# Kernel optimization log

Hardware: AMD Instinct MI355X
Metric: run time of the kernel (lower is better)

## Reference

```python
import jax, jax.numpy as jnp
import numpy as np

LN_EPS = 1e-5


def _ln(x, g, b):
    m = jnp.mean(x, axis=-1, keepdims=True)
    v = jnp.mean((x - m) ** 2, axis=-1, keepdims=True)
    return (x - m) / jnp.sqrt(v + LN_EPS) * g + b


def setup_inputs() -> dict:
    key = jax.random.key(0)
    ks = jax.random.split(key, 8)
    B, N, S, D, T = 16, 64, 2048, 1024, 768

    def xavier(k, shape):
        fan_in, fan_out = shape
        lim = (6.0 / (fan_in + fan_out)) ** 0.5
        return jax.random.uniform(k, shape, minval=-lim, maxval=lim, dtype=jnp.float32)

    return {
        "prev_states": jax.random.normal(ks[0], (B, N, D), dtype=jnp.float32),
        "input_tokens": jax.random.normal(ks[1], (B, S, T), dtype=jnp.float32),
        # input_projection (token_dim -> state_dim)
        "W_proj": xavier(ks[2], (T, D)),
        "b_proj": jnp.zeros((D,), jnp.float32),
        # three LayerNorms
        "g_state": jnp.ones((D,), jnp.float32), "beta_state": jnp.zeros((D,), jnp.float32),
        "g_input": jnp.ones((D,), jnp.float32), "beta_input": jnp.zeros((D,), jnp.float32),
        "g_out": jnp.ones((D,), jnp.float32), "beta_out": jnp.zeros((D,), jnp.float32),
        # GRU gates (2D -> D); update-gate bias initialized to -1 as in the module
        "W_u": xavier(ks[3], (2 * D, D)), "b_u": jnp.full((D,), -1.0, jnp.float32),
        "W_r": xavier(ks[4], (2 * D, D)), "b_r": jnp.zeros((D,), jnp.float32),
        "W_n": xavier(ks[5], (2 * D, D)), "b_n": jnp.zeros((D,), jnp.float32),
    }


def reference(prev_states, input_tokens, W_proj, b_proj,
              g_state, beta_state, g_input, beta_input, g_out, beta_out,
              W_u, b_u, W_r, b_r, W_n, b_n):
    D = prev_states.shape[-1]
    # project tokens to state dim: (B,S,D)
    tok = input_tokens @ W_proj + b_proj
    # attention routing (routing_weights=None path)
    scores = jnp.einsum('bnd,bsd->bns', prev_states, tok) / jnp.sqrt(jnp.float32(D))
    attn = jax.nn.softmax(scores, axis=-1)
    routed = jnp.einsum('bns,bsd->bnd', attn, tok)  # (B,N,D)
    # GRU-style gated update, vectorized over the num_states axis
    ps_n = _ln(prev_states, g_state, beta_state)
    in_n = _ln(routed, g_input, beta_input)
    concat = jnp.concatenate([ps_n, in_n], axis=-1)  # (B,N,2D)
    u = jax.nn.sigmoid(concat @ W_u + b_u)
    r = jax.nn.sigmoid(concat @ W_r + b_r)
    reset_in = jnp.concatenate([r * ps_n, in_n], axis=-1)
    cand = jnp.tanh(reset_in @ W_n + b_n)  # dropout is identity in eval
    new_state = (1.0 - u) * prev_states + u * cand
    return _ln(new_state, g_out, beta_out)
```

## Files before the change

### kernel.cpp

```cpp
#include <hip/hip_runtime.h>
#include <stdint.h>

typedef __attribute__((ext_vector_type(4))) float floatx4;
typedef __attribute__((ext_vector_type(8))) short shortx8;

#define LN_EPS 1e-5f

__device__ __forceinline__ unsigned short f2b(float f) {
  unsigned u = __builtin_bit_cast(unsigned, f);
  u = (u + 0x7FFFu + ((u >> 16) & 1u)) >> 16;
  return (unsigned short)u;
}
__device__ __forceinline__ float b2f(unsigned short h) {
  return __builtin_bit_cast(float, (unsigned)h << 16);
}

__device__ __forceinline__ void g2l16(const unsigned short* g, unsigned short* l) {
  __builtin_amdgcn_global_load_lds(
      (const __attribute__((address_space(1))) unsigned int*)g,
      (__attribute__((address_space(3))) unsigned int*)l, 16, 0, 0);
}

__device__ __forceinline__ float wave_sum(float v) {
#pragma unroll
  for (int o = 32; o; o >>= 1) v += __shfl_down(v, o, 64);
  return v;
}
__device__ __forceinline__ float block_sum(float v, float* s) {
  v = wave_sum(v);
  __syncthreads();
  if ((threadIdx.x & 63) == 0) s[threadIdx.x >> 6] = v;
  __syncthreads();
  return s[0] + s[1] + s[2] + s[3];
}

__global__ __launch_bounds__(256) void k_transpose4(
    const float* __restrict__ Wu, const float* __restrict__ Wr,
    const float* __restrict__ Wn, const float* __restrict__ Wp,
    unsigned short* __restrict__ Wtur, unsigned short* __restrict__ Wtn,
    unsigned short* __restrict__ Wtp) {
  __shared__ float tile[32][33];
  const int which = blockIdx.z;
  const float* in;
  unsigned short* out;
  int K;
  if (which == 0)      { in = Wu; out = Wtur;              K = 2048; }
  else if (which == 1) { in = Wr; out = Wtur + 1024 * 2048; K = 2048; }
  else if (which == 2) { in = Wn; out = Wtn;               K = 2048; }
  else                 { in = Wp; out = Wtp;               K = 768;  }
  const int N = 1024;
  const int k0 = blockIdx.x * 32, n0 = blockIdx.y * 32;
  if (k0 >= K) return;
  const int tx = threadIdx.x & 31, ty = threadIdx.x >> 5;
#pragma unroll
  for (int i = 0; i < 32; i += 8)
    tile[ty + i][tx] = in[(long)(k0 + ty + i) * N + n0 + tx];
  __syncthreads();
#pragma unroll
  for (int i = 0; i < 32; i += 8)
    out[(long)(n0 + ty + i) * K + k0 + tx] = f2b(tile[tx][ty + i]);
}

__global__ __launch_bounds__(256) void k_cvt3(
    const float* __restrict__ prev, unsigned short* __restrict__ psb,
    const float* __restrict__ toks, unsigned short* __restrict__ tokb,
    const float* __restrict__ wp, unsigned short* __restrict__ wpb,
    float* __restrict__ rs) {
  if (blockIdx.x == 0) {
    floatx4 z = {0.f, 0.f, 0.f, 0.f};
    *(floatx4*)(rs + threadIdx.x * 4) = z;
  }
  const long chunk = (long)blockIdx.x * 256 + threadIdx.x;
  const float* src;
  unsigned short* dst;
  long i;
  if (chunk < 262144) { src = prev; dst = psb; i = chunk * 4; }
  else if (chunk < 6553600) { src = toks; dst = tokb; i = (chunk - 262144) * 4; }
  else { src = wp; dst = wpb; i = (chunk - 6553600) * 4; }
  floatx4 v = *(const floatx4*)(src + i);
  unsigned short t4[4];
#pragma unroll
  for (int j = 0; j < 4; j++) t4[j] = f2b(v[j]);
  *(uint2*)(dst + i) = *(uint2*)t4;
}

__global__ __launch_bounds__(256) void k_gemm64(
    const unsigned short* __restrict__ A, long sAb, int lda,
    const unsigned short* __restrict__ Bt, long sBb, int ldb,
    int K,
    const float* __restrict__ bias, const float* __restrict__ bias2,
    float scale, int mode,
    void* __restrict__ out, int ldc, long sCb,
    unsigned short* __restrict__ out2,
    const unsigned short* __restrict__ aux_psn,
    const float* __restrict__ aux_u, const float* __restrict__ aux_prev,
    float* __restrict__ rs) {
  __shared__ unsigned short As[2][64 * 64];
  __shared__ unsigned short Bs[2][64 * 64];
  const int tid = threadIdx.x;
  const int wave = tid >> 6, lane = tid & 63;
  const int b = blockIdx.z;
  const int m0 = blockIdx.x * 64, n0 = blockIdx.y * 64;
  const int wm = wave & 1, wn = wave >> 1;
  const int l16 = lane & 15, quad = lane >> 4;
  const int srow8 = lane >> 3;
  const int c8 = ((lane & 7) ^ srow8) * 8;
  const unsigned short* Ab = A + (long)b * sAb;
  const unsigned short* Bb = Bt + (long)b * sBb;

  const unsigned short* gA[2];
  const unsigned short* gB[2];
  int lAoff[2], lBoff[2];
#pragma unroll
  for (int j = 0; j < 2; j++) {
    const int rb = wave * 16 + j * 8;
    gA[j] = Ab + (long)(m0 + rb + srow8) * lda + c8;
    gB[j] = Bb + (long)(n0 + rb + srow8) * ldb + c8;
    lAoff[j] = rb * 64;
    lBoff[j] = rb * 64;
  }
  int offA[2][2], offB[2][2];
#pragma unroll
  for (int ks = 0; ks < 2; ks++)
#pragma unroll
    for (int i = 0; i < 2; i++) {
      int r = wm * 32 + i * 16 + l16;
      offA[ks][i] = r * 64 + (((ks * 4 + quad) ^ (r & 7)) * 8);
      r = wn * 32 + i * 16 + l16;
      offB[ks][i] = r * 64 + (((ks * 4 + quad) ^ (r & 7)) * 8);
    }

  floatx4 acc[2][2] = {};

#pragma unroll
  for (int j = 0; j < 2; j++) {
    g2l16(gA[j], &As[0][lAoff[j]]);
    g2l16(gB[j], &Bs[0][lBoff[j]]);
  }
  __syncthreads();

  const int nt = K >> 6;
  for (int t = 0; t < nt; t++) {
    const int cur = t & 1;
    if (t + 1 < nt) {
      const int kn = (t + 1) << 6;
#pragma unroll
      for (int j = 0; j < 2; j++) {
        g2l16(gA[j] + kn, &As[cur ^ 1][lAoff[j]]);
        g2l16(gB[j] + kn, &Bs[cur ^ 1][lBoff[j]]);
      }
    }
#pragma unroll
    for (int ks = 0; ks < 2; ks++) {
      shortx8 af[2], bf[2];
#pragma unroll
      for (int i = 0; i < 2; i++) af[i] = *(const shortx8*)&As[cur][offA[ks][i]];
#pragma unroll
      for (int j = 0; j < 2; j++) bf[j] = *(const shortx8*)&Bs[cur][offB[ks][j]];
#pragma unroll
      for (int i = 0; i < 2; i++)
#pragma unroll
        for (int j = 0; j < 2; j++)
          acc[i][j] = __builtin_amdgcn_mfma_f32_16x16x32_bf16(af[i], bf[j], acc[i][j], 0, 0, 0);
    }
    __syncthreads();
  }

  if (mode == 0) {
#pragma unroll
    for (int i = 0; i < 2; i++) {
      float psum[4] = {0.f, 0.f, 0.f, 0.f};
#pragma unroll
      for (int j = 0; j < 2; j++) {
        const int rbase = m0 + wm * 32 + i * 16 + quad * 4;
        const int c = n0 + wn * 32 + j * 16 + l16;
#pragma unroll
        for (int r = 0; r < 4; r++) {
          const float e = expf(acc[i][j][r] * scale);
          out2[(long)b * sCb + (long)(rbase + r) * ldc + c] = f2b(e);
          psum[r] += e;
        }
      }
#pragma unroll
      for (int r = 0; r < 4; r++) {
        float s = psum[r];
        s += __shfl_xor(s, 1, 64);
        s += __shfl_xor(s, 2, 64);
        s += __shfl_xor(s, 4, 64);
        s += __shfl_xor(s, 8, 64);
        if (l16 == 0)
          atomicAdd(rs + (long)b * 64 + m0 + wm * 32 + i * 16 + quad * 4 + r, s);
      }
    }
    return;
  }

#pragma unroll
  for (int i = 0; i < 2; i++)
#pragma unroll
    for (int j = 0; j < 2; j++) {
      const int rbase = m0 + wm * 32 + i * 16 + quad * 4;
      const int c = n0 + wn * 32 + j * 16 + l16;
      float bval = 0.0f;
      if (bias) bval = (mode == 5 && c >= 1024) ? bias2[c - 1024] : bias[c];
#pragma unroll
      for (int r = 0; r < 4; r++) {
        const int row = rbase + r;
        float v = acc[i][j][r] * scale + bval;
        const long cidx = (long)b * sCb + (long)row * ldc + c;
        if (mode == 1) {
          out2[cidx] = f2b(v);
        } else if (mode == 3) {
          float cand = tanhf(v);
          float u = aux_u[(long)row * 1024 + c];
          float p = aux_prev[(long)row * 1024 + c];
          ((float*)out)[cidx] = (1.0f - u) * p + u * cand;
        } else if (mode == 6) {
          ((float*)out)[cidx] = v + aux_u[row] * bias2[c];
        } else {
          if (c < 1024) {
            ((float*)out)[(long)row * 1024 + c] = 1.0f / (1.0f + expf(-v));
          } else {
            const int cc = c - 1024;
            float rr = 1.0f / (1.0f + expf(-v));
            out2[(long)row * 2048 + cc] = f2b(rr * b2f(aux_psn[(long)row * 2048 + cc]));
          }
        }
      }
    }
}

__global__ __launch_bounds__(256) void k_routed_mfma(
    const unsigned short* __restrict__ attnb,
    const unsigned short* __restrict__ tok,
    float* __restrict__ parts) {
  __shared__ unsigned short As[64 * 40];
  __shared__ unsigned short Bs[32 * 66];
  const int kc = blockIdx.x, nt = blockIdx.y, b = blockIdx.z;
  const int tid = threadIdx.x;
  const int wave = tid >> 6, lane = tid & 63;
  const int wm = wave & 1, wn = wave >> 1;
  const int l16 = lane & 15, quad = lane >> 4;
  const int n0 = nt * 64;
  const long abase = (long)b * 131072 + (long)kc * 1024;
  const long tbase = ((long)b * 2048 + (long)kc * 1024) * 768;
  const int srow = tid >> 2, skc = (tid & 3) * 8;
  const int bk = tid >> 3, bd = (tid & 7) * 8;

  floatx4 acc[2][2] = {};

  uint4 pa = *(const uint4*)(attnb + abase + (long)srow * 2048 + skc);
  uint4 pb = *(const uint4*)(tok + tbase + (long)bk * 768 + n0 + bd);

  for (int k0 = 0; k0 < 1024; k0 += 32) {
    *(uint4*)&As[srow * 40 + skc] = pa;
    {
      const unsigned* pv = (const unsigned*)&pb;
      unsigned short* dst = &Bs[bk * 66 + bd];
#pragma unroll
      for (int w2 = 0; w2 < 4; w2++) *(unsigned*)(dst + w2 * 2) = pv[w2];
    }
    if (k0 + 32 < 1024) {
      pa = *(const uint4*)(attnb + abase + (long)srow * 2048 + (k0 + 32) + skc);
      pb = *(const uint4*)(tok + tbase + (long)(k0 + 32 + bk) * 768 + n0 + bd);
    }
    asm volatile("s_waitcnt lgkmcnt(0)" ::: "memory");
    __builtin_amdgcn_s_barrier();
    __builtin_amdgcn_sched_barrier(0);

    shortx8 a0 = *(const shortx8*)&As[(wm * 32 + 0  + l16) * 40 + quad * 8];
    shortx8 a1 = *(const shortx8*)&As[(wm * 32 + 16 + l16) * 40 + quad * 8];
    shortx8 b0, b1;
#pragma unroll
    for (int j = 0; j < 8; j++) {
      b0[j] = *(const short*)&Bs[(quad * 8 + j) * 66 + wn * 32 + l16];
      b1[j] = *(const short*)&Bs[(quad * 8 + j) * 66 + wn * 32 + 16 + l16];
    }
    acc[0][0] = __builtin_amdgcn_mfma_f32_16x16x32_bf16(a0, b0, acc[0][0], 0, 0, 0);
    acc[0][1] = __builtin_amdgcn_mfma_f32_16x16x32_bf16(a0, b1, acc[0][1], 0, 0, 0);
    acc[1][0] = __builtin_amdgcn_mfma_f32_16x16x32_bf16(a1, b0, acc[1][0], 0, 0, 0);
    acc[1][1] = __builtin_amdgcn_mfma_f32_16x16x32_bf16(a1, b1, acc[1][1], 0, 0, 0);
    __builtin_amdgcn_s_barrier();
  }

#pragma unroll
  for (int im = 0; im < 2; im++)
#pragma unroll
    for (int in_ = 0; in_ < 2; in_++) {
      const int rbase = wm * 32 + im * 16 + quad * 4;
      const int c = n0 + wn * 32 + in_ * 16 + l16;
#pragma unroll
      for (int r = 0; r < 4; r++)
        parts[(long)kc * 786432 + ((long)b * 64 + rbase + r) * 768 + c] =
            acc[im][in_][r];
    }
}

__global__ __launch_bounds__(256) void k_sumcvt(
    const float* __restrict__ parts, unsigned short* __restrict__ out) {
  const long i = ((long)blockIdx.x * 256 + threadIdx.x) * 4;
  floatx4 v = *(const floatx4*)(parts + i);
  floatx4 w = *(const floatx4*)(parts + 786432 + i);
  unsigned short t4[4];
#pragma unroll
  for (int j = 0; j < 4; j++) t4[j] = f2b(v[j] + w[j]);
  *(uint2*)(out + i) = *(uint2*)t4;
}

__global__ __launch_bounds__(256) void k_ln2(
    const float* __restrict__ prev, const float* __restrict__ routed,
    const float* __restrict__ g_st, const float* __restrict__ be_st,
    const float* __restrict__ g_in, const float* __restrict__ be_in,
    unsigned short* __restrict__ conc, unsigned short* __restrict__ candA) {
  __shared__ float scr[4];
  const long r = blockIdx.x & 1023;
  const bool second = blockIdx.x >= 1024;
  const int t = threadIdx.x;
  floatx4 v;
  const float *g, *be;
  if (!second) {
    v = *(const floatx4*)(prev + r * 1024 + t * 4);
    g = g_st; be = be_st;
  } else {
    v = *(const floatx4*)(routed + r * 1024 + t * 4);
    g = g_in; be = be_in;
  }
  float s1 = v[0] + v[1] + v[2] + v[3];
  float s2 = v[0] * v[0] + v[1] * v[1] + v[2] * v[2] + v[3] * v[3];
  s1 = block_sum(s1, scr);
  s2 = block_sum(s2, scr);
  const float mean = s1 * (1.0f / 1024.0f);
  const float var = s2 * (1.0f / 1024.0f) - mean * mean;
  const float rstd = rsqrtf(var + LN_EPS);
#pragma unroll
  for (int i = 0; i < 4; i++) {
    const int d = t * 4 + i;
    const float y = (v[i] - mean) * rstd * g[d] + be[d];
    const unsigned short h = f2b(y);
    if (!second) {
      conc[r * 2048 + d] = h;
    } else {
      conc[r * 2048 + 1024 + d] = h;
      candA[r * 2048 + 1024 + d] = h;
    }
  }
}

__global__ __launch_bounds__(256) void k_ln_out(
    const float* __restrict__ in, const float* __restrict__ g,
    const float* __restrict__ be, float* __restrict__ out) {
  __shared__ float scr[4];
  const long r = blockIdx.x;
  const int t = threadIdx.x;
  floatx4 v = *(const floatx4*)(in + r * 1024 + t * 4);
  float s1 = v[0] + v[1] + v[2] + v[3];
  float s2 = v[0] * v[0] + v[1] * v[1] + v[2] * v[2] + v[3] * v[3];
  s1 = block_sum(s1, scr);
  s2 = block_sum(s2, scr);
  const float mean = s1 * (1.0f / 1024.0f);
  const float var = s2 * (1.0f / 1024.0f) - mean * mean;
  const float rstd = rsqrtf(var + LN_EPS);
  floatx4 o;
#pragma unroll
  for (int i = 0; i < 4; i++) {
    const int d = t * 4 + i;
    o[i] = (v[i] - mean) * rstd * g[d] + be[d];
  }
  *(floatx4*)(out + r * 1024 + t * 4) = o;
}

extern "C" void kernel_launch(void* const* d_in, const int* in_sizes, int n_in,
                              void* d_out, int out_size, void* d_ws, size_t ws_size,
                              hipStream_t stream) {
  (void)in_sizes; (void)n_in; (void)out_size; (void)ws_size;
  const float* prev  = (const float*)d_in[0];
  const float* toks  = (const float*)d_in[1];
  const float* Wp    = (const float*)d_in[2];
  const float* bp    = (const float*)d_in[3];
  const float* g_st  = (const float*)d_in[4];
  const float* be_st = (const float*)d_in[5];
  const float* g_in  = (const float*)d_in[6];
  const float* be_in = (const float*)d_in[7];
  const float* g_o   = (const float*)d_in[8];
  const float* be_o  = (const float*)d_in[9];
  const float* Wu    = (const float*)d_in[10];
  const float* bu    = (const float*)d_in[11];
  const float* Wr    = (const float*)d_in[12];
  const float* br    = (const float*)d_in[13];
  const float* Wn    = (const float*)d_in[14];
  const float* bn    = (const float*)d_in[15];
  float* out = (float*)d_out;

  char* ws = (char*)d_ws;
  unsigned short* tokb  = (unsigned short*)ws; ws += 50331648;
  unsigned short* psb   = (unsigned short*)ws; ws += 2097152;
  unsigned short* Wpb   = (unsigned short*)ws; ws += 1572864;
  unsigned short* Wtp   = (unsigned short*)ws; ws += 1572864;
  unsigned short* pwb   = (unsigned short*)ws; ws += 1572864;
  unsigned short* attnb = (unsigned short*)ws; ws += 4194304;
  float*          rowsum= (float*)ws;          ws += 4096;
  float*          parts = (float*)ws;          ws += 6291456;
  unsigned short* rwb   = (unsigned short*)ws; ws += 1572864;
  float*          routed= (float*)ws;          ws += 4194304;
  unsigned short* conc  = (unsigned short*)ws; ws += 4194304;
  unsigned short* candA = (unsigned short*)ws; ws += 4194304;
  float*          ubuf  = (float*)ws;          ws += 4194304;
  float*          ns    = (float*)ws;          ws += 4194304;
  unsigned short* Wtur  = (unsigned short*)ws; ws += 8388608;
  unsigned short* Wtn   = (unsigned short*)ws; ws += 4194304;

  const dim3 blk(256);

  k_cvt3<<<dim3(26368), blk, 0, stream>>>(prev, psb, toks, tokb, Wp, Wpb, rowsum);
  k_transpose4<<<dim3(64, 32, 4), blk, 0, stream>>>(Wu, Wr, Wn, Wp, Wtur, Wtn, Wtp);
  k_gemm64<<<dim3(16, 12, 1), blk, 0, stream>>>(
      psb, 0L, 1024, Wpb, 0L, 1024, 1024,
      nullptr, nullptr, 1.0f, 1,
      nullptr, 768, 0L, pwb, nullptr, nullptr, nullptr, nullptr);
  k_gemm64<<<dim3(1, 32, 16), blk, 0, stream>>>(
      pwb, 49152L, 768, tokb, 1572864L, 768, 768,
      nullptr, nullptr, 0.03125f, 0,
      nullptr, 2048, 131072L, attnb, nullptr, nullptr, nullptr, rowsum);
  k_routed_mfma<<<dim3(2, 12, 16), blk, 0, stream>>>(attnb, tokb, parts);
  k_sumcvt<<<dim3(768), blk, 0, stream>>>(parts, rwb);
  k_gemm64<<<dim3(16, 16, 1), blk, 0, stream>>>(
      rwb, 0L, 768, Wtp, 0L, 768, 768,
      nullptr, bp, 1.0f, 6,
      (void*)routed, 1024, 0L, nullptr, nullptr, rowsum, nullptr, nullptr);
  k_ln2<<<dim3(2048), blk, 0, stream>>>(prev, routed, g_st, be_st, g_in, be_in,
                                        conc, candA);
  k_gemm64<<<dim3(16, 32, 1), blk, 0, stream>>>(
      conc, 0L, 2048, Wtur, 0L, 2048, 2048,
      bu, br, 1.0f, 5,
      (void*)ubuf, 1024, 0L, candA, conc, nullptr, nullptr, nullptr);
  k_gemm64<<<dim3(16, 16, 1), blk, 0, stream>>>(
      candA, 0L, 2048, Wtn, 0L, 2048, 2048,
      bn, nullptr, 1.0f, 3,
      (void*)ns, 1024, 0L, nullptr, nullptr, ubuf, prev, nullptr);
  k_ln_out<<<dim3(1024), blk, 0, stream>>>(ns, g_o, be_o, out);
}
```

Before: 330.9 us.

## Merge prep kernels, use 128x128 GEMM tiles, drop split-K routed reduction

The conversion and weight-transpose kernels are merged into one launch. The dense GEMMs move from 64x64 to 128x128 tiles with a 4x4 MFMA accumulator per wave. The routed attention GEMM now runs the full K=2048 in one block and writes bf16 directly, which removes the partial-sum buffer and the k_sumcvt launch. The intent is fewer launches and more data reuse per block, but the 128-tile GEMMs launch only 48 to 128 blocks on a GPU with many CUs, and the routed kernel halves its block count, so occupancy may suffer.

```diff
diff --git a/kernel.cpp b/kernel.cpp
--- a/kernel.cpp
+++ b/kernel.cpp
@@ -34,23 +34,57 @@
   return s[0] + s[1] + s[2] + s[3];
 }
 
-__global__ __launch_bounds__(256) void k_transpose4(
+__global__ __launch_bounds__(256) void k_prep(
+    const float* __restrict__ prev, unsigned short* __restrict__ psb,
+    const float* __restrict__ toks, unsigned short* __restrict__ tokb,
+    const float* __restrict__ wp, unsigned short* __restrict__ wpb,
     const float* __restrict__ Wu, const float* __restrict__ Wr,
-    const float* __restrict__ Wn, const float* __restrict__ Wp,
+    const float* __restrict__ Wn,
     unsigned short* __restrict__ Wtur, unsigned short* __restrict__ Wtn,
-    unsigned short* __restrict__ Wtp) {
+    unsigned short* __restrict__ Wtp, float* __restrict__ rs) {
   __shared__ float tile[32][33];
-  const int which = blockIdx.z;
+  const int bid = blockIdx.x;
+  if (bid < 26368) {
+    if (bid == 0) {
+      floatx4 z = {0.f, 0.f, 0.f, 0.f};
+      *(floatx4*)(rs + threadIdx.x * 4) = z;
+    }
+    const long chunk = (long)bid * 256 + threadIdx.x;
+    const float* src;
+    unsigned short* dst;
+    long i;
+    if (chunk < 262144) { src = prev; dst = psb; i = chunk * 4; }
+    else if (chunk < 6553600) { src = toks; dst = tokb; i = (chunk - 262144) * 4; }
+    else { src = wp; dst = wpb; i = (chunk - 6553600) * 4; }
+    floatx4 v = *(const floatx4*)(src + i);
+    unsigned short t4[4];
+#pragma unroll
+    for (int j = 0; j < 4; j++) t4[j] = f2b(v[j]);
+    *(uint2*)(dst + i) = *(uint2*)t4;
+    return;
+  }
+  int t = bid - 26368;
   const float* in;
   unsigned short* out;
-  int K;
-  if (which == 0)      { in = Wu; out = Wtur;              K = 2048; }
-  else if (which == 1) { in = Wr; out = Wtur + 1024 * 2048; K = 2048; }
-  else if (which == 2) { in = Wn; out = Wtn;               K = 2048; }
-  else                 { in = Wp; out = Wtp;               K = 768;  }
+  int K, kx, ny;
+  if (t < 6144) {
+    const int which = t >> 11;
+    const int t2 = t & 2047;
+    kx = t2 & 63;
+    ny = t2 >> 6;
+    K = 2048;
+    in = which == 0 ? Wu : (which == 1 ? Wr : Wn);
+    out = which == 0 ? Wtur : (which == 1 ? Wtur + 1024 * 2048 : Wtn);
+  } else {
+    const int t2 = t - 6144;
+    kx = t2 % 24;
+    ny = t2 / 24;
+    K = 768;
+    in = wp;
+    out = Wtp;
+  }
   const int N = 1024;
-  const int k0 = blockIdx.x * 32, n0 = blockIdx.y * 32;
-  if (k0 >= K) return;
+  const int k0 = kx * 32, n0 = ny * 32;
   const int tx = threadIdx.x & 31, ty = threadIdx.x >> 5;
 #pragma unroll
   for (int i = 0; i < 32; i += 8)
@@ -61,39 +95,122 @@
     out[(long)(n0 + ty + i) * K + k0 + tx] = f2b(tile[tx][ty + i]);
 }
 
-__global__ __launch_bounds__(256) void k_cvt3(
-    const float* __restrict__ prev, unsigned short* __restrict__ psb,
-    const float* __restrict__ toks, unsigned short* __restrict__ tokb,
-    const float* __restrict__ wp, unsigned short* __restrict__ wpb,
-    float* __restrict__ rs) {
-  if (blockIdx.x == 0) {
-    floatx4 z = {0.f, 0.f, 0.f, 0.f};
-    *(floatx4*)(rs + threadIdx.x * 4) = z;
-  }
-  const long chunk = (long)blockIdx.x * 256 + threadIdx.x;
-  const float* src;
-  unsigned short* dst;
-  long i;
-  if (chunk < 262144) { src = prev; dst = psb; i = chunk * 4; }
-  else if (chunk < 6553600) { src = toks; dst = tokb; i = (chunk - 262144) * 4; }
-  else { src = wp; dst = wpb; i = (chunk - 6553600) * 4; }
-  floatx4 v = *(const floatx4*)(src + i);
-  unsigned short t4[4];
-#pragma unroll
-  for (int j = 0; j < 4; j++) t4[j] = f2b(v[j]);
-  *(uint2*)(dst + i) = *(uint2*)t4;
-}
-
-__global__ __launch_bounds__(256) void k_gemm64(
+__global__ __launch_bounds__(256) void k_gemm128(
+    const unsigned short* __restrict__ A, int lda,
+    const unsigned short* __restrict__ Bt, int ldb,
+    int K,
+    const float* __restrict__ bias, const float* __restrict__ bias2,
+    int mode,
+    void* __restrict__ out, int ldc,
+    unsigned short* __restrict__ out2,
+    const unsigned short* __restrict__ aux_psn,
+    const float* __restrict__ aux_u, const float* __restrict__ aux_prev) {
+  __shared__ unsigned short As[2][128 * 64];
+  __shared__ unsigned short Bs[2][128 * 64];
+  const int tid = threadIdx.x;
+  const int wave = tid >> 6, lane = tid & 63;
+  const int m0 = blockIdx.x * 128, n0 = blockIdx.y * 128;
+  const int wm = wave & 1, wn = wave >> 1;
+  const int l16 = lane & 15, quad = lane >> 4;
+  const int srow8 = lane >> 3;
+  const int c8 = ((lane & 7) ^ srow8) * 8;
+
+  const unsigned short* gA[4];
+  const unsigned short* gB[4];
+  int lOff[4];
+#pragma unroll
+  for (int j = 0; j < 4; j++) {
+    const int rb = wave * 32 + j * 8;
+    gA[j] = A + (long)(m0 + rb + srow8) * lda + c8;
+    gB[j] = Bt + (long)(n0 + rb + srow8) * ldb + c8;
+    lOff[j] = rb * 64;
+  }
+  int offA[2][4], offB[2][4];
+#pragma unroll
+  for (int ks = 0; ks < 2; ks++)
+#pragma unroll
+    for (int i = 0; i < 4; i++) {
+      int r = wm * 64 + i * 16 + l16;
+      offA[ks][i] = r * 64 + (((ks * 4 + quad) ^ (r & 7)) * 8);
+      r = wn * 64 + i * 16 + l16;
+      offB[ks][i] = r * 64 + (((ks * 4 + quad) ^ (r & 7)) * 8);
+    }
+
+  floatx4 acc[4][4] = {};
+
+#pragma unroll
+  for (int j = 0; j < 4; j++) {
+    g2l16(gA[j], &As[0][lOff[j]]);
+    g2l16(gB[j], &Bs[0][lOff[j]]);
+  }
+  __syncthreads();
+
+  const int nt = K >> 6;
+  for (int t = 0; t < nt; t++) {
+    const int cur = t & 1;
+    if (t + 1 < nt) {
+      const int kn = (t + 1) << 6;
+#pragma unroll
+      for (int j = 0; j < 4; j++) {
+        g2l16(gA[j] + kn, &As[cur ^ 1][lOff[j]]);
+        g2l16(gB[j] + kn, &Bs[cur ^ 1][lOff[j]]);
+      }
+    }
+#pragma unroll
+    for (int ks = 0; ks < 2; ks++) {
+      shortx8 af[4], bf[4];
+#pragma unroll
+      for (int i = 0; i < 4; i++) af[i] = *(const shortx8*)&As[cur][offA[ks][i]];
+#pragma unroll
+      for (int j = 0; j < 4; j++) bf[j] = *(const shortx8*)&Bs[cur][offB[ks][j]];
+#pragma unroll
+      for (int i = 0; i < 4; i++)
+#pragma unroll
+        for (int j = 0; j < 4; j++)
+          acc[i][j] = __builtin_amdgcn_mfma_f32_16x16x32_bf16(af[i], bf[j], acc[i][j], 0, 0, 0);
+    }
+    __syncthreads();
+  }
+
+#pragma unroll
+  for (int i = 0; i < 4; i++)
+#pragma unroll
+    for (int j = 0; j < 4; j++) {
+      const int rbase = m0 + wm * 64 + i * 16 + quad * 4;
+      const int c = n0 + wn * 64 + j * 16 + l16;
+      float bval = 0.0f;
+      if (bias) bval = (mode == 5 && c >= 1024) ? bias2[c - 1024] : bias[c];
+#pragma unroll
+      for (int r = 0; r < 4; r++) {
+        const int row = rbase + r;
+        float v = acc[i][j][r] + bval;
+        if (mode == 1) {
+          out2[(long)row * ldc + c] = f2b(v);
+        } else if (mode == 3) {
+          float cand = tanhf(v);
+          float u = aux_u[(long)row * 1024 + c];
+          float p = aux_prev[(long)row * 1024 + c];
+          ((float*)out)[(long)row * ldc + c] = (1.0f - u) * p + u * cand;
+        } else if (mode == 6) {
+          ((float*)out)[(long)row * ldc + c] = v + aux_u[row] * bias2[c];
+        } else {
+          if (c < 1024) {
+            ((float*)out)[(long)row * 1024 + c] = 1.0f / (1.0f + expf(-v));
+          } else {
+            const int cc = c - 1024;
+            float rr = 1.0f / (1.0f + expf(-v));
+            out2[(long)row * 2048 + cc] = f2b(rr * b2f(aux_psn[(long)row * 2048 + cc]));
+          }
+        }
+      }
+    }
+}
+
+__global__ __launch_bounds__(256) void k_scores(
     const unsigned short* __restrict__ A, long sAb, int lda,
     const unsigned short* __restrict__ Bt, long sBb, int ldb,
-    int K,
-    const float* __restrict__ bias, const float* __restrict__ bias2,
-    float scale, int mode,
-    void* __restrict__ out, int ldc, long sCb,
-    unsigned short* __restrict__ out2,
-    const unsigned short* __restrict__ aux_psn,
-    const float* __restrict__ aux_u, const float* __restrict__ aux_prev,
+    int K, float scale,
+    unsigned short* __restrict__ out2, int ldc, long sCb,
     float* __restrict__ rs) {
   __shared__ unsigned short As[2][64 * 64];
   __shared__ unsigned short Bs[2][64 * 64];
@@ -110,14 +227,13 @@
 
   const unsigned short* gA[2];
   const unsigned short* gB[2];
-  int lAoff[2], lBoff[2];
+  int lOff[2];
 #pragma unroll
   for (int j = 0; j < 2; j++) {
     const int rb = wave * 16 + j * 8;
     gA[j] = Ab + (long)(m0 + rb + srow8) * lda + c8;
     gB[j] = Bb + (long)(n0 + rb + srow8) * ldb + c8;
-    lAoff[j] = rb * 64;
-    lBoff[j] = rb * 64;
+    lOff[j] = rb * 64;
   }
   int offA[2][2], offB[2][2];
 #pragma unroll
@@ -134,8 +250,8 @@
 
 #pragma unroll
   for (int j = 0; j < 2; j++) {
-    g2l16(gA[j], &As[0][lAoff[j]]);
-    g2l16(gB[j], &Bs[0][lBoff[j]]);
+    g2l16(gA[j], &As[0][lOff[j]]);
+    g2l16(gB[j], &Bs[0][lOff[j]]);
   }
   __syncthreads();
 
@@ -146,8 +262,8 @@
       const int kn = (t + 1) << 6;
 #pragma unroll
       for (int j = 0; j < 2; j++) {
-        g2l16(gA[j] + kn, &As[cur ^ 1][lAoff[j]]);
-        g2l16(gB[j] + kn, &Bs[cur ^ 1][lBoff[j]]);
+        g2l16(gA[j] + kn, &As[cur ^ 1][lOff[j]]);
+        g2l16(gB[j] + kn, &Bs[cur ^ 1][lOff[j]]);
       }
     }
 #pragma unroll
@@ -166,84 +282,47 @@
     __syncthreads();
   }
 
-  if (mode == 0) {
-#pragma unroll
-    for (int i = 0; i < 2; i++) {
-      float psum[4] = {0.f, 0.f, 0.f, 0.f};
-#pragma unroll
-      for (int j = 0; j < 2; j++) {
-        const int rbase = m0 + wm * 32 + i * 16 + quad * 4;
-        const int c = n0 + wn * 32 + j * 16 + l16;
-#pragma unroll
-        for (int r = 0; r < 4; r++) {
-          const float e = expf(acc[i][j][r] * scale);
-          out2[(long)b * sCb + (long)(rbase + r) * ldc + c] = f2b(e);
-          psum[r] += e;
-        }
-      }
-#pragma unroll
-      for (int r = 0; r < 4; r++) {
-        float s = psum[r];
-        s += __shfl_xor(s, 1, 64);
-        s += __shfl_xor(s, 2, 64);
-        s += __shfl_xor(s, 4, 64);
-        s += __shfl_xor(s, 8, 64);
-        if (l16 == 0)
-          atomicAdd(rs + (long)b * 64 + m0 + wm * 32 + i * 16 + quad * 4 + r, s);
-      }
-    }
-    return;
-  }
-
-#pragma unroll
-  for (int i = 0; i < 2; i++)
+#pragma unroll
+  for (int i = 0; i < 2; i++) {
+    float psum[4] = {0.f, 0.f, 0.f, 0.f};
 #pragma unroll
     for (int j = 0; j < 2; j++) {
       const int rbase = m0 + wm * 32 + i * 16 + quad * 4;
       const int c = n0 + wn * 32 + j * 16 + l16;
-      float bval = 0.0f;
-      if (bias) bval = (mode == 5 && c >= 1024) ? bias2[c - 1024] : bias[c];
 #pragma unroll
       for (int r = 0; r < 4; r++) {
-        const int row = rbase + r;
-        float v = acc[i][j][r] * scale + bval;
-        const long cidx = (long)b * sCb + (long)row * ldc + c;
-        if (mode == 1) {
-          out2[cidx] = f2b(v);
-        } else if (mode == 3) {
-          float cand = tanhf(v);
-          float u = aux_u[(long)row * 1024 + c];
-          float p = aux_prev[(long)row * 1024 + c];
-          ((float*)out)[cidx] = (1.0f - u) * p + u * cand;
-        } else if (mode == 6) {
-          ((float*)out)[cidx] = v + aux_u[row] * bias2[c];
-        } else {
-          if (c < 1024) {
-            ((float*)out)[(long)row * 1024 + c] = 1.0f / (1.0f + expf(-v));
-          } else {
-            const int cc = c - 1024;
-            float rr = 1.0f / (1.0f + expf(-v));
-            out2[(long)row * 2048 + cc] = f2b(rr * b2f(aux_psn[(long)row * 2048 + cc]));
-          }
-        }
+        const float e = expf(acc[i][j][r] * scale);
+        out2[(long)b * sCb + (long)(rbase + r) * ldc + c] = f2b(e);
+        psum[r] += e;
       }
     }
+#pragma unroll
+    for (int r = 0; r < 4; r++) {
+      float s = psum[r];
+      s += __shfl_xor(s, 1, 64);
+      s += __shfl_xor(s, 2, 64);
+      s += __shfl_xor(s, 4, 64);
+      s += __shfl_xor(s, 8, 64);
+      if (l16 == 0)
+        atomicAdd(rs + (long)b * 64 + m0 + wm * 32 + i * 16 + quad * 4 + r, s);
+    }
+  }
 }
 
 __global__ __launch_bounds__(256) void k_routed_mfma(
     const unsigned short* __restrict__ attnb,
     const unsigned short* __restrict__ tok,
-    float* __restrict__ parts) {
+    unsigned short* __restrict__ rwb) {
   __shared__ unsigned short As[64 * 40];
   __shared__ unsigned short Bs[32 * 66];
-  const int kc = blockIdx.x, nt = blockIdx.y, b = blockIdx.z;
+  const int nt = blockIdx.x, b = blockIdx.y;
   const int tid = threadIdx.x;
   const int wave = tid >> 6, lane = tid & 63;
   const int wm = wave & 1, wn = wave >> 1;
   const int l16 = lane & 15, quad = lane >> 4;
   const int n0 = nt * 64;
-  const long abase = (long)b * 131072 + (long)kc * 1024;
-  const long tbase = ((long)b * 2048 + (long)kc * 1024) * 768;
+  const long abase = (long)b * 131072;
+  const long tbase = (long)b * 1572864;
   const int srow = tid >> 2, skc = (tid & 3) * 8;
   const int bk = tid >> 3, bd = (tid & 7) * 8;
 
@@ -252,7 +331,7 @@
   uint4 pa = *(const uint4*)(attnb + abase + (long)srow * 2048 + skc);
   uint4 pb = *(const uint4*)(tok + tbase + (long)bk * 768 + n0 + bd);
 
-  for (int k0 = 0; k0 < 1024; k0 += 32) {
+  for (int k0 = 0; k0 < 2048; k0 += 32) {
     *(uint4*)&As[srow * 40 + skc] = pa;
     {
       const unsigned* pv = (const unsigned*)&pb;
@@ -260,7 +339,7 @@
 #pragma unroll
       for (int w2 = 0; w2 < 4; w2++) *(unsigned*)(dst + w2 * 2) = pv[w2];
     }
-    if (k0 + 32 < 1024) {
+    if (k0 + 32 < 2048) {
       pa = *(const uint4*)(attnb + abase + (long)srow * 2048 + (k0 + 32) + skc);
       pb = *(const uint4*)(tok + tbase + (long)(k0 + 32 + bk) * 768 + n0 + bd);
     }
@@ -291,20 +370,8 @@
       const int c = n0 + wn * 32 + in_ * 16 + l16;
 #pragma unroll
       for (int r = 0; r < 4; r++)
-        parts[(long)kc * 786432 + ((long)b * 64 + rbase + r) * 768 + c] =
-            acc[im][in_][r];
-    }
-}
-
-__global__ __launch_bounds__(256) void k_sumcvt(
-    const float* __restrict__ parts, unsigned short* __restrict__ out) {
-  const long i = ((long)blockIdx.x * 256 + threadIdx.x) * 4;
-  floatx4 v = *(const floatx4*)(parts + i);
-  floatx4 w = *(const floatx4*)(parts + 786432 + i);
-  unsigned short t4[4];
-#pragma unroll
-  for (int j = 0; j < 4; j++) t4[j] = f2b(v[j] + w[j]);
-  *(uint2*)(out + i) = *(uint2*)t4;
+        rwb[((long)b * 64 + rbase + r) * 768 + c] = f2b(acc[im][in_][r]);
+    }
 }
 
 __global__ __launch_bounds__(256) void k_ln2(
@@ -399,7 +466,6 @@
   unsigned short* pwb   = (unsigned short*)ws; ws += 1572864;
   unsigned short* attnb = (unsigned short*)ws; ws += 4194304;
   float*          rowsum= (float*)ws;          ws += 4096;
-  float*          parts = (float*)ws;          ws += 6291456;
   unsigned short* rwb   = (unsigned short*)ws; ws += 1572864;
   float*          routed= (float*)ws;          ws += 4194304;
   unsigned short* conc  = (unsigned short*)ws; ws += 4194304;
@@ -411,31 +477,29 @@
 
   const dim3 blk(256);
 
-  k_cvt3<<<dim3(26368), blk, 0, stream>>>(prev, psb, toks, tokb, Wp, Wpb, rowsum);
-  k_transpose4<<<dim3(64, 32, 4), blk, 0, stream>>>(Wu, Wr, Wn, Wp, Wtur, Wtn, Wtp);
-  k_gemm64<<<dim3(16, 12, 1), blk, 0, stream>>>(
-      psb, 0L, 1024, Wpb, 0L, 1024, 1024,
-      nullptr, nullptr, 1.0f, 1,
-      nullptr, 768, 0L, pwb, nullptr, nullptr, nullptr, nullptr);
-  k_gemm64<<<dim3(1, 32, 16), blk, 0, stream>>>(
-      pwb, 49152L, 768, tokb, 1572864L, 768, 768,
-      nullptr, nullptr, 0.03125f, 0,
-      nullptr, 2048, 131072L, attnb, nullptr, nullptr, nullptr, rowsum);
-  k_routed_mfma<<<dim3(2, 12, 16), blk, 0, stream>>>(attnb, tokb, parts);
-  k_sumcvt<<<dim3(768), blk, 0, stream>>>(parts, rwb);
-  k_gemm64<<<dim3(16, 16, 1), blk, 0, stream>>>(
-      rwb, 0L, 768, Wtp, 0L, 768, 768,
-      nullptr, bp, 1.0f, 6,
-      (void*)routed, 1024, 0L, nullptr, nullptr, rowsum, nullptr, nullptr);
+  k_prep<<<dim3(33280), blk, 0, stream>>>(prev, psb, toks, tokb, Wp, Wpb,
+                                          Wu, Wr, Wn, Wtur, Wtn, Wtp, rowsum);
+  k_gemm128<<<dim3(8, 6), blk, 0, stream>>>(
+      psb, 1024, Wpb, 1024, 1024,
+      nullptr, nullptr, 1,
+      nullptr, 768, pwb, nullptr, nullptr, nullptr);
+  k_scores<<<dim3(1, 32, 16), blk, 0, stream>>>(
+      pwb, 49152L, 768, tokb, 1572864L, 768, 768, 0.03125f,
+      attnb, 2048, 131072L, rowsum);
+  k_routed_mfma<<<dim3(12, 16), blk, 0, stream>>>(attnb, tokb, rwb);
+  k_gemm128<<<dim3(8, 8), blk, 0, stream>>>(
+      rwb, 768, Wtp, 768, 768,
+      nullptr, bp, 6,
+      (void*)routed, 1024, nullptr, nullptr, rowsum, nullptr);
   k_ln2<<<dim3(2048), blk, 0, stream>>>(prev, routed, g_st, be_st, g_in, be_in,
                                         conc, candA);
-  k_gemm64<<<dim3(16, 32, 1), blk, 0, stream>>>(
-      conc, 0L, 2048, Wtur, 0L, 2048, 2048,
-      bu, br, 1.0f, 5,
-      (void*)ubuf, 1024, 0L, candA, conc, nullptr, nullptr, nullptr);
-  k_gemm64<<<dim3(16, 16, 1), blk, 0, stream>>>(
-      candA, 0L, 2048, Wtn, 0L, 2048, 2048,
-      bn, nullptr, 1.0f, 3,
-      (void*)ns, 1024, 0L, nullptr, nullptr, ubuf, prev, nullptr);
+  k_gemm128<<<dim3(8, 16), blk, 0, stream>>>(
+      conc, 2048, Wtur, 2048, 2048,
+      bu, br, 5,
+      (void*)ubuf, 1024, candA, conc, nullptr, nullptr);
+  k_gemm128<<<dim3(8, 8), blk, 0, stream>>>(
+      candA, 2048, Wtn, 2048, 2048,
+      bn, nullptr, 3,
+      (void*)ns, 1024, nullptr, nullptr, ubuf, prev);
   k_ln_out<<<dim3(1024), blk, 0, stream>>>(ns, g_o, be_o, out);
 }
```

New measurement: 432.3 us. 30.7% more time.
